# Optimization experiments

Hardware: AMD Instinct MI355X
Metric: run time of the kernel (lower is better)

Reference implementation:

```python
import jax, jax.numpy as jnp
import numpy as np

EMB = 256   # EMB_SIZE hard-coded in source
H = 8       # num heads (all heads share the same Q/K/V, as in source)
DK = EMB // H  # 32
B, T = 16, 2048
LN_EPS = 1e-5


def _layernorm(a, g, b):
    m = jnp.mean(a, axis=-1, keepdims=True)
    v = jnp.mean(jnp.square(a - m), axis=-1, keepdims=True)
    return (a - m) * jax.lax.rsqrt(v + LN_EPS) * g + b


def setup_inputs() -> dict:
    key = jax.random.key(0)
    ks = jax.random.split(key, 8)
    sc = 0.02
    return {
        "x": jax.random.normal(ks[0], (B, T, EMB), jnp.float32),
        "Wq": jax.random.normal(ks[1], (EMB, DK), jnp.float32) * sc,
        "Wk": jax.random.normal(ks[2], (EMB, DK), jnp.float32) * sc,
        "Wv": jax.random.normal(ks[3], (EMB, DK), jnp.float32) * sc,
        "Wp": jax.random.normal(ks[4], (EMB, EMB), jnp.float32) * sc,
        "bp": jnp.zeros((EMB,), jnp.float32),
        "W1": jax.random.normal(ks[5], (EMB, 4 * EMB), jnp.float32) * sc,
        "b1": jnp.zeros((4 * EMB,), jnp.float32),
        "W2": jax.random.normal(ks[6], (4 * EMB, EMB), jnp.float32) * sc,
        "b2": jnp.zeros((EMB,), jnp.float32),
        "g1": jnp.ones((EMB,), jnp.float32),
        "be1": jnp.zeros((EMB,), jnp.float32),
        "g2": jnp.ones((EMB,), jnp.float32),
        "be2": jnp.zeros((EMB,), jnp.float32),
    }


def reference(x, Wq, Wk, Wv, Wp, bp, W1, b1, W2, b2, g1, be1, g2, be2):
    # Single shared-head QKV projections (bias-free), as in source
    q = x @ Wq  # [B,T,DK]
    k = x @ Wk
    v = x @ Wv
    # Causal self-attention with explicit score matrix [B,T,T]
    scores = jnp.einsum("btd,bsd->bts", q, k) / jnp.sqrt(jnp.float32(DK))
    causal = jnp.tril(jnp.ones((T, T), dtype=bool))
    scores = jnp.where(causal, scores, -jnp.inf)
    a = jax.nn.softmax(scores, axis=-1)
    attn = jnp.einsum("bts,bsd->btd", a, v)  # [B,T,DK]
    # Source concatenates h identical copies of the same attention output
    cat = jnp.tile(attn, (1, 1, H))  # [B,T,EMB]
    mh = cat @ Wp + bp
    y1 = _layernorm(x + mh, g1, be1)
    ff = jax.nn.gelu(y1 @ W1 + b1, approximate=False) @ W2 + b2
    return _layernorm(y1 + ff, g2, be2)
```

## Files before the change

### kernel.cpp

```cpp
#include <hip/hip_runtime.h>

#define BB 16
#define TT 2048
#define EE 256
#define DK 32
#define MM (BB*TT)
#define FF 1024

typedef __bf16 bf16_t;
typedef __bf16 bf16x8 __attribute__((ext_vector_type(8)));
typedef __bf16 bf16x4 __attribute__((ext_vector_type(4)));
typedef float  f32x4  __attribute__((ext_vector_type(4)));

__device__ __forceinline__ f32x4 mfma16(bf16x8 a, bf16x8 b, f32x4 c){
  return __builtin_amdgcn_mfma_f32_16x16x32_bf16(a, b, c, 0, 0, 0);
}
__device__ __forceinline__ void gload_lds16(const void* g, void* l){
  __builtin_amdgcn_global_load_lds((__attribute__((address_space(1))) void*)g,
                                   (__attribute__((address_space(3))) void*)l,
                                   16, 0, 0);
}

__launch_bounds__(256)
__global__ void prep_kernel(const float* __restrict__ Wq, const float* __restrict__ Wk,
                            const float* __restrict__ Wv, const float* __restrict__ Wp,
                            const float* __restrict__ W1, const float* __restrict__ W2,
                            bf16_t* __restrict__ wqkv, float* __restrict__ wpe,
                            bf16_t* __restrict__ w1t, bf16_t* __restrict__ w2t)
{
  const int i = blockIdx.x*256 + threadIdx.x;
  if (i < 96*256) {
    const int r = i >> 8, c = i & 255;
    float v;
    if (r < 32)      v = Wq[c*32 + r] * 0.17677669529663687f;
    else if (r < 64) v = Wk[c*32 + (r-32)];
    else             v = Wv[c*32 + (r-64)];
    wqkv[i] = (bf16_t)v;
  }
  if (i < 32*256) {
    const int d = i >> 8, n = i & 255;
    float s = 0.f;
    #pragma unroll
    for (int h = 0; h < 8; ++h) s += Wp[(h*32 + d)*256 + n];
    wpe[i] = s;
  }
  if (i < 1024*256) {
    const int n = i >> 8, k = i & 255;
    w1t[i] = (bf16_t)W1[(size_t)k*1024 + n];
  }
  if (i < 256*1024) {
    const int n = i >> 10, k = i & 1023;
    w2t[i] = (bf16_t)W2[(size_t)k*256 + n];
  }
}

__launch_bounds__(256)
__global__ void qkv_kernel(const float* __restrict__ x, const bf16_t* __restrict__ wqkv,
                           bf16_t* __restrict__ q, bf16_t* __restrict__ kd,
                           bf16_t* __restrict__ vT)
{
  __shared__ bf16_t Ws[96*256];
  bf16_t* Vt = Ws;
  const int tid = threadIdx.x;
  #pragma unroll
  for (int i = 0; i < 12; ++i) {
    const int v8  = tid + i*256;
    const int row = v8 >> 5;
    const int bir = (v8 & 31) * 16;
    *(bf16x8*)((char*)Ws + row*512 + (bir ^ ((row & 7) << 4))) =
        *(const bf16x8*)(wqkv + (size_t)v8*8);
  }
  __syncthreads();

  const int w = tid >> 6, l = tid & 63;
  const int lr = l & 15, lk4 = l >> 4, lkb = lk4*8;
  const int m0 = blockIdx.x * 64;
  const int arow = m0 + w*16 + lr;
  const float* xr = x + (size_t)arow * 256;

  f32x4 acc[6] = {};
  #pragma unroll
  for (int s = 0; s < 8; ++s) {
    const int kb = s*32 + lkb;
    const float4 v0 = *(const float4*)(xr + kb);
    const float4 v1 = *(const float4*)(xr + kb + 4);
    bf16x8 a;
    a[0]=(bf16_t)v0.x; a[1]=(bf16_t)v0.y; a[2]=(bf16_t)v0.z; a[3]=(bf16_t)v0.w;
    a[4]=(bf16_t)v1.x; a[5]=(bf16_t)v1.y; a[6]=(bf16_t)v1.z; a[7]=(bf16_t)v1.w;
    #pragma unroll
    for (int j = 0; j < 6; ++j) {
      const int nrow = j*16 + lr;
      const bf16x8 bf = *(const bf16x8*)((const char*)Ws + nrow*512 +
                                         ((kb*2) ^ ((nrow & 7) << 4)));
      acc[j] = mfma16(a, bf, acc[j]);
    }
  }
  #pragma unroll
  for (int j = 0; j < 4; ++j) {
    #pragma unroll
    for (int r = 0; r < 4; ++r) {
      const int orow = m0 + w*16 + lk4*4 + r;
      const int col  = j*16 + lr;
      const bf16_t v = (bf16_t)acc[j][r];
      if (col < 32) q[(size_t)orow*32 + col] = v;
      else          kd[(size_t)orow*32 + (col-32)] = v;
    }
  }
  __syncthreads();
  #pragma unroll
  for (int j = 4; j < 6; ++j)
    #pragma unroll
    for (int r = 0; r < 4; ++r) {
      const int d = (j-4)*16 + lr;
      const int t = w*16 + lk4*4 + r;
      *(bf16_t*)((char*)Vt + d*128 + ((((t>>3) ^ (d&7))<<4) | ((t&7)*2))) =
          (bf16_t)acc[j][r];
    }
  __syncthreads();
  {
    const int d = tid >> 3, c8 = tid & 7;
    const bf16x8 v = *(const bf16x8*)((char*)Vt + d*128 + ((c8 ^ (d&7))<<4));
    *(bf16x8*)(vT + ((size_t)(m0 >> 11)*32 + d)*TT + (m0 & 2047) + c8*8) = v;
  }
}

__launch_bounds__(256)
__global__ void attnp_kernel(const bf16_t* __restrict__ q, const bf16_t* __restrict__ kd,
                             const bf16_t* __restrict__ vT,
                             float* __restrict__ part_acc, float* __restrict__ part_ml)
{
  __shared__ bf16_t P[4][16*128];
  const int tid = threadIdx.x;
  const int w = tid >> 6, l = tid & 63;
  const int wv = blockIdx.x*4 + w;
  const int lr = l & 15, g4 = l >> 4;
  const float NEG_INF = -__builtin_inff();

  const int b = wv / 320;
  const int u = wv - b*320;
  int r, base;
  if      (u >= 192) { r = 3; base = 192; }
  else if (u >= 96)  { r = 2; base = 96;  }
  else if (u >= 32)  { r = 1; base = 32;  }
  else               { r = 0; base = 0;   }
  const int qq = u - base;
  const int g  = r*32 + qq / (r+1);
  const int c  = qq - (qq / (r+1))*(r+1);
  const int t_total = (g >> 3) + 1;
  const int t0 = c*4;
  const int t1 = min(t0 + 4, t_total);

  const bf16_t* qb = q  + (size_t)b*TT*32;
  const bf16_t* kb = kd + (size_t)b*TT*32;
  const bf16_t* vb = vT + (size_t)b*32*TT;
  const int q0 = g*16;
  const int qg = q0 + lr;

  const bf16x8 qa = *(const bf16x8*)(qb + (size_t)(q0 + lr)*32 + g4*8);
  const bf16_t* v0r = vb + (size_t)lr*TT;
  const bf16_t* v1r = vb + (size_t)(16 + lr)*TT;

  f32x4 acc0 = {0.f,0.f,0.f,0.f}, acc1 = {0.f,0.f,0.f,0.f};
  float mrun = NEG_INF, lsum = 0.f;
  char* pb = (char*)&P[w][0];
  const int swz = (lr & 7) << 4;
  const f32x4 zf = {0.f,0.f,0.f,0.f};

  for (int t = t0; t < t1; ++t) {
    const int k0 = t * 128;
    f32x4 s[8];
    #pragma unroll
    for (int cc = 0; cc < 8; ++cc) {
      const bf16x8 kf = *(const bf16x8*)(kb + (size_t)(k0 + cc*16 + lr)*32 + g4*8);
      s[cc] = mfma16(kf, qa, zf);
    }
    if (t == t_total - 1) {
      #pragma unroll
      for (int cc = 0; cc < 8; ++cc)
        #pragma unroll
        for (int rr = 0; rr < 4; ++rr)
          if (k0 + cc*16 + g4*4 + rr > qg) s[cc][rr] = NEG_INF;
    }
    float mt = NEG_INF;
    #pragma unroll
    for (int cc = 0; cc < 8; ++cc) {
      float a01 = fmaxf(s[cc][0], s[cc][1]), a23 = fmaxf(s[cc][2], s[cc][3]);
      mt = fmaxf(mt, fmaxf(a01, a23));
    }
    mt = fmaxf(mt, __shfl_xor(mt, 16));
    mt = fmaxf(mt, __shfl_xor(mt, 32));
    const float mn = fmaxf(mrun, mt);
    const float sc = __expf(mrun - mn);
    float ps = 0.f;
    #pragma unroll
    for (int cc = 0; cc < 8; ++cc) {
      float p0 = __expf(s[cc][0]-mn), p1 = __expf(s[cc][1]-mn);
      float p2 = __expf(s[cc][2]-mn), p3 = __expf(s[cc][3]-mn);
      s[cc][0]=p0; s[cc][1]=p1; s[cc][2]=p2; s[cc][3]=p3;
      ps += (p0+p1) + (p2+p3);
    }
    ps += __shfl_xor(ps, 16);
    ps += __shfl_xor(ps, 32);
    lsum = lsum*sc + ps;
    mrun = mn;
    acc0 *= sc; acc1 *= sc;
    #pragma unroll
    for (int cc = 0; cc < 8; ++cc) {
      bf16x4 pk;
      pk[0]=(bf16_t)s[cc][0]; pk[1]=(bf16_t)s[cc][1];
      pk[2]=(bf16_t)s[cc][2]; pk[3]=(bf16_t)s[cc][3];
      *(bf16x4*)(pb + lr*256 + ((cc*32 + g4*8) ^ swz)) = pk;
    }
    #pragma unroll
    for (int h = 0; h < 4; ++h) {
      const bf16x8 pbf = *(const bf16x8*)(pb + lr*256 + ((h*64 + g4*16) ^ swz));
      acc0 = mfma16(*(const bf16x8*)(v0r + k0 + h*32 + g4*8), pbf, acc0);
      acc1 = mfma16(*(const bf16x8*)(v1r + k0 + h*32 + g4*8), pbf, acc1);
    }
  }
  float* pa = part_acc + (size_t)wv*512;
  *(f32x4*)(pa + l*8)     = acc0;
  *(f32x4*)(pa + l*8 + 4) = acc1;
  if (l < 16) {
    part_ml[wv*32 + l]      = mrun;
    part_ml[wv*32 + 16 + l] = lsum;
  }
}

__launch_bounds__(256)
__global__ void attnc_kernel(const float* __restrict__ part_acc,
                             const float* __restrict__ part_ml,
                             bf16_t* __restrict__ attn)
{
  const int tid = threadIdx.x;
  const int id = blockIdx.x*4 + (tid >> 6);
  const int l = tid & 63, lr = l & 15, g4 = l >> 4;
  const int b = id >> 7, g = id & 127;
  const int r = g >> 5;
  const int base = (r == 0) ? 0 : (r == 1) ? 32 : (r == 2) ? 96 : 192;
  const int p0 = b*320 + base + (g - (r << 5))*(r + 1);
  const int nc = r + 1;
  const float NEG_INF = -__builtin_inff();

  float m0v=NEG_INF,m1v=NEG_INF,m2v=NEG_INF,m3v=NEG_INF;
  float l0v=0,l1v=0,l2v=0,l3v=0;
  f32x4 a00={0,0,0,0},a01={0,0,0,0},a10={0,0,0,0},a11={0,0,0,0};
  f32x4 a20={0,0,0,0},a21={0,0,0,0},a30={0,0,0,0},a31={0,0,0,0};
  {
    const float* pa = part_acc + (size_t)p0*512;
    a00 = *(const f32x4*)(pa + l*8); a01 = *(const f32x4*)(pa + l*8 + 4);
    m0v = part_ml[p0*32 + lr]; l0v = part_ml[p0*32 + 16 + lr];
  }
  if (nc > 1) {
    const float* pa = part_acc + (size_t)(p0+1)*512;
    a10 = *(const f32x4*)(pa + l*8); a11 = *(const f32x4*)(pa + l*8 + 4);
    m1v = part_ml[(p0+1)*32 + lr]; l1v = part_ml[(p0+1)*32 + 16 + lr];
  }
  if (nc > 2) {
    const float* pa = part_acc + (size_t)(p0+2)*512;
    a20 = *(const f32x4*)(pa + l*8); a21 = *(const f32x4*)(pa + l*8 + 4);
    m2v = part_ml[(p0+2)*32 + lr]; l2v = part_ml[(p0+2)*32 + 16 + lr];
  }
  if (nc > 3) {
    const float* pa = part_acc + (size_t)(p0+3)*512;
    a30 = *(const f32x4*)(pa + l*8); a31 = *(const f32x4*)(pa + l*8 + 4);
    m3v = part_ml[(p0+3)*32 + lr]; l3v = part_ml[(p0+3)*32 + 16 + lr];
  }
  const float M = fmaxf(fmaxf(m0v, m1v), fmaxf(m2v, m3v));
  const float w0 = __expf(m0v - M), w1 = __expf(m1v - M);
  const float w2 = __expf(m2v - M), w3 = __expf(m3v - M);
  const float L = l0v*w0 + l1v*w1 + l2v*w2 + l3v*w3;
  const float inv = 1.0f / L;
  f32x4 o0 = (a00*w0 + a10*w1 + a20*w2 + a30*w3) * inv;
  f32x4 o1 = (a01*w0 + a11*w1 + a21*w2 + a31*w3) * inv;

  bf16_t* ao = attn + ((size_t)b*TT + g*16 + lr)*32;
  bf16x4 ob0, ob1;
  ob0[0]=(bf16_t)o0[0]; ob0[1]=(bf16_t)o0[1]; ob0[2]=(bf16_t)o0[2]; ob0[3]=(bf16_t)o0[3];
  ob1[0]=(bf16_t)o1[0]; ob1[1]=(bf16_t)o1[1]; ob1[2]=(bf16_t)o1[2]; ob1[3]=(bf16_t)o1[3];
  *(bf16x4*)(ao + g4*4)      = ob0;
  *(bf16x4*)(ao + 16 + g4*4) = ob1;
}

__launch_bounds__(256)
__global__ void ln1_kernel(const float* __restrict__ x, const bf16_t* __restrict__ attn,
                           const float* __restrict__ wpe, const float* __restrict__ bp,
                           const float* __restrict__ g1, const float* __restrict__ be1,
                           bf16_t* __restrict__ y1b)
{
  __shared__ float Wp_s[32*256];
  const int tid = threadIdx.x;
  for (int i = tid; i < 32*64; i += 256)
    ((float4*)Wp_s)[i] = ((const float4*)wpe)[i];
  __syncthreads();

  const int w = tid >> 6, l = tid & 63;
  const int n = l * 4;
  const float4 gv  = *(const float4*)(g1  + n);
  const float4 bev = *(const float4*)(be1 + n);
  const float4 bpv = *(const float4*)(bp  + n);

  #pragma unroll 1
  for (int it = 0; it < 8; ++it) {
    const int row = blockIdx.x*32 + it*4 + w;
    const bf16_t* ar = attn + (size_t)row*32;
    float a[32];
    #pragma unroll
    for (int i = 0; i < 4; ++i) {
      const bf16x8 t = *(const bf16x8*)(ar + i*8);
      #pragma unroll
      for (int j = 0; j < 8; ++j) a[i*8 + j] = (float)t[j];
    }
    float mh[4] = {bpv.x, bpv.y, bpv.z, bpv.w};
    #pragma unroll
    for (int d = 0; d < 32; ++d) {
      const float4 wv = *(const float4*)(Wp_s + d*256 + n);
      const float ad = a[d];
      mh[0] = fmaf(ad, wv.x, mh[0]); mh[1] = fmaf(ad, wv.y, mh[1]);
      mh[2] = fmaf(ad, wv.z, mh[2]); mh[3] = fmaf(ad, wv.w, mh[3]);
    }
    const float4 xv = *(const float4*)(x + (size_t)row*256 + n);
    const float t0 = xv.x + mh[0], t1 = xv.y + mh[1];
    const float t2 = xv.z + mh[2], t3 = xv.w + mh[3];
    float s1 = (t0+t1) + (t2+t3);
    float s2 = (t0*t0 + t1*t1) + (t2*t2 + t3*t3);
    #pragma unroll
    for (int m = 1; m < 64; m <<= 1) { s1 += __shfl_xor(s1, m); s2 += __shfl_xor(s2, m); }
    const float mean = s1 * (1.0f/256.0f);
    const float var  = s2 * (1.0f/256.0f) - mean*mean;
    const float rs   = rsqrtf(var + 1e-5f);
    float4 yv;
    yv.x = (t0-mean)*rs*gv.x + bev.x; yv.y = (t1-mean)*rs*gv.y + bev.y;
    yv.z = (t2-mean)*rs*gv.z + bev.z; yv.w = (t3-mean)*rs*gv.w + bev.w;
    bf16x4 yb; yb[0]=(bf16_t)yv.x; yb[1]=(bf16_t)yv.y; yb[2]=(bf16_t)yv.z; yb[3]=(bf16_t)yv.w;
    *(bf16x4*)(y1b + (size_t)row*256 + n) = yb;
  }
}

__launch_bounds__(512, 1)
__global__ void mlp_kernel(const bf16_t* __restrict__ y1b, const bf16_t* __restrict__ w1t,
                           const float* __restrict__ b1, const bf16_t* __restrict__ w2t,
                           const float* __restrict__ b2, const float* __restrict__ g2,
                           const float* __restrict__ be2, float* __restrict__ out)
{
  __shared__ char SM[135168];
  const int tid = threadIdx.x;
  const int w = tid >> 6, l = tid & 63;
  const int lr = l & 15, g4 = l >> 4;
  const int m0 = blockIdx.x * 128;
  const int rw = w & 3;
  const int cw = w >> 2;
  const int wm  = rw * 32;
  const int wn1 = cw * 16;
  const int wn2 = cw * 128;

  {
    const float2 bv = *(const float2*)(b1 + tid*2);
    *(float2*)(SM + 131072 + tid*8) = bv;
  }
  bf16x8 aA[2][8];
  #pragma unroll
  for (int t = 0; t < 2; ++t)
    #pragma unroll
    for (int kk = 0; kk < 8; ++kk)
      aA[t][kk] = *(const bf16x8*)(y1b +
          (size_t)(m0 + wm + t*16 + lr)*256 + kk*32 + g4*8);
  asm volatile("s_waitcnt vmcnt(0) lgkmcnt(0)" ::: "memory");
  __builtin_amdgcn_sched_barrier(0);

  #define ST_W1(c, s)                                                         \
    { _Pragma("unroll")                                                       \
      for (int p_ = 0; p_ < 2; ++p_) {                                        \
        const int idx_ = p_*512 + tid;                                        \
        const int r_ = idx_ >> 5, c_ = idx_ & 31;                             \
        const int sc_ = (c_ & 24) | ((c_ ^ r_) & 7);                          \
        gload_lds16(w1t + (size_t)((c)*32 + r_)*256 + sc_*8,                  \
                    SM + (s)*16384 + idx_*16);                                \
      } }
  #define ST_W2(c, s)                                                         \
    { _Pragma("unroll")                                                       \
      for (int p_ = 0; p_ < 2; ++p_) {                                        \
        const int idx_ = p_*512 + tid;                                        \
        const int r_ = idx_ >> 2, c_ = idx_ & 3;                              \
        gload_lds16(w2t + (size_t)r_*1024 + (c)*32 + ((c_ ^ r_) & 3)*8,       \
                    SM + 49152 + (s)*16384 + idx_*16);                        \
      } }

  ST_W1(0, 0);
  ST_W1(1, 1);
  ST_W2(0, 0);

  f32x4 oacc[2][8] = {};

  #pragma unroll 1
  for (int i = 0; i < 32; ++i) {
    if (i < 31) { asm volatile("s_waitcnt vmcnt(4)" ::: "memory"); }
    else        { asm volatile("s_waitcnt vmcnt(2)" ::: "memory"); }
    __builtin_amdgcn_sched_barrier(0);
    asm volatile("s_waitcnt lgkmcnt(0)" ::: "memory");
    __builtin_amdgcn_sched_barrier(0);
    __builtin_amdgcn_s_barrier();
    __builtin_amdgcn_sched_barrier(0);

    const char* sw1 = SM + (i % 3)*16384;
    f32x4 ah[2] = {};
    const int nr = wn1 + lr;
    __builtin_amdgcn_s_setprio(1);
    #pragma unroll
    for (int kk = 0; kk < 8; ++kk) {
      const bf16x8 bf = *(const bf16x8*)(sw1 + nr*512 +
                                         ((kk*64 + g4*16) ^ ((nr & 7) << 4)));
      ah[0] = mfma16(aA[0][kk], bf, ah[0]);
      ah[1] = mfma16(aA[1][kk], bf, ah[1]);
    }
    if (i > 0) {
      const char* sw2 = SM + 49152 + ((i-1) % 3)*16384;
      const char* hs  = SM + 98304 + ((i-1) & 1)*16384;
      bf16x8 ha[2], wb[8];
      #pragma unroll
      for (int i3 = 0; i3 < 2; ++i3) {
        const int row = wm + i3*16 + lr;
        ha[i3] = *(const bf16x8*)(hs + row*128 + ((g4*16) ^ ((row & 7) << 4)));
      }
      #pragma unroll
      for (int j3 = 0; j3 < 8; ++j3) {
        const int n = wn2 + j3*16 + lr;
        wb[j3] = *(const bf16x8*)(sw2 + n*64 + ((g4*16) ^ ((n & 3) << 4)));
      }
      #pragma unroll
      for (int i3 = 0; i3 < 2; ++i3)
        #pragma unroll
        for (int j3 = 0; j3 < 8; ++j3)
          oacc[i3][j3] = mfma16(ha[i3], wb[j3], oacc[i3][j3]);
    }
    __builtin_amdgcn_s_setprio(0);
    {
      const float bias = *(const float*)(SM + 131072 + (i*32 + wn1 + lr)*4);
      char* hw = SM + 98304 + (i & 1)*16384;
      const int hc2 = (wn1 + lr)*2;
      #pragma unroll
      for (int i3 = 0; i3 < 2; ++i3)
        #pragma unroll
        for (int r = 0; r < 4; ++r) {
          const int hrow = wm + i3*16 + g4*4 + r;
          const float v = ah[i3][r] + bias;
          const float z = 1.5957691216057308f * v * fmaf(0.044715f, v*v, 1.0f);
          const float gg = v * __builtin_amdgcn_rcpf(1.0f + __expf(-z));
          *(bf16_t*)(hw + hrow*128 + (hc2 ^ ((hrow & 7) << 4))) = (bf16_t)gg;
        }
    }
    if (i <= 29) ST_W1(i+2, (i+2) % 3);
    if (i <= 30) ST_W2(i+1, (i+1) % 3);
  }
  #undef ST_W1
  #undef ST_W2

  asm volatile("s_waitcnt vmcnt(0)" ::: "memory");
  __builtin_amdgcn_sched_barrier(0);
  asm volatile("s_waitcnt lgkmcnt(0)" ::: "memory");
  __builtin_amdgcn_sched_barrier(0);
  __builtin_amdgcn_s_barrier();
  __builtin_amdgcn_sched_barrier(0);
  {
    const char* sw2 = SM + 49152 + (31 % 3)*16384;
    const char* hs  = SM + 98304 + (31 & 1)*16384;
    bf16x8 ha[2], wb[8];
    #pragma unroll
    for (int i3 = 0; i3 < 2; ++i3) {
      const int row = wm + i3*16 + lr;
      ha[i3] = *(const bf16x8*)(hs + row*128 + ((g4*16) ^ ((row & 7) << 4)));
    }
    #pragma unroll
    for (int j3 = 0; j3 < 8; ++j3) {
      const int n = wn2 + j3*16 + lr;
      wb[j3] = *(const bf16x8*)(sw2 + n*64 + ((g4*16) ^ ((n & 3) << 4)));
    }
    #pragma unroll
    for (int i3 = 0; i3 < 2; ++i3)
      #pragma unroll
      for (int j3 = 0; j3 < 8; ++j3)
        oacc[i3][j3] = mfma16(ha[i3], wb[j3], oacc[i3][j3]);
  }

  float b2r[8], g2r[8], be2r[8];
  #pragma unroll
  for (int j3 = 0; j3 < 8; ++j3) {
    const int col = wn2 + j3*16 + lr;
    b2r[j3] = b2[col]; g2r[j3] = g2[col]; be2r[j3] = be2[col];
  }
  #pragma unroll
  for (int i3 = 0; i3 < 2; ++i3)
    #pragma unroll
    for (int r = 0; r < 4; ++r) {
      const int grow = m0 + wm + i3*16 + g4*4 + r;
      #pragma unroll
      for (int j3 = 0; j3 < 8; ++j3) {
        const int col = wn2 + j3*16 + lr;
        oacc[i3][j3][r] += b2r[j3] + (float)y1b[(size_t)grow*256 + col];
      }
    }
  __syncthreads();
  float* red = (float*)SM;
  #pragma unroll
  for (int i3 = 0; i3 < 2; ++i3)
    #pragma unroll
    for (int r = 0; r < 4; ++r) {
      float s1 = 0.f, s2 = 0.f;
      #pragma unroll
      for (int j3 = 0; j3 < 8; ++j3) {
        s1 += oacc[i3][j3][r]; s2 += oacc[i3][j3][r]*oacc[i3][j3][r];
      }
      #pragma unroll
      for (int m = 1; m < 16; m <<= 1) { s1 += __shfl_xor(s1, m); s2 += __shfl_xor(s2, m); }
      if (lr == 0) {
        const int rl = wm + i3*16 + g4*4 + r;
        red[rl*4 + cw*2]     = s1;
        red[rl*4 + cw*2 + 1] = s2;
      }
    }
  __syncthreads();
  #pragma unroll
  for (int i3 = 0; i3 < 2; ++i3)
    #pragma unroll
    for (int r = 0; r < 4; ++r) {
      const int rl = wm + i3*16 + g4*4 + r;
      const float S1 = red[rl*4+0] + red[rl*4+2];
      const float S2 = red[rl*4+1] + red[rl*4+3];
      const float mean = S1 * (1.0f/256.0f);
      const float var  = S2 * (1.0f/256.0f) - mean*mean;
      const float rs   = rsqrtf(var + 1e-5f);
      #pragma unroll
      for (int j3 = 0; j3 < 8; ++j3) {
        const int col = wn2 + j3*16 + lr;
        out[(size_t)(m0 + rl)*256 + col] = (oacc[i3][j3][r] - mean)*rs*g2r[j3] + be2r[j3];
      }
    }
}

extern "C" void kernel_launch(void* const* d_in, const int* in_sizes, int n_in,
                              void* d_out, int out_size, void* d_ws, size_t ws_size,
                              hipStream_t stream)
{
  const float* x   = (const float*)d_in[0];
  const float* Wq  = (const float*)d_in[1];
  const float* Wk  = (const float*)d_in[2];
  const float* Wv  = (const float*)d_in[3];
  const float* Wp  = (const float*)d_in[4];
  const float* bp  = (const float*)d_in[5];
  const float* W1  = (const float*)d_in[6];
  const float* b1  = (const float*)d_in[7];
  const float* W2  = (const float*)d_in[8];
  const float* b2  = (const float*)d_in[9];
  const float* g1  = (const float*)d_in[10];
  const float* be1 = (const float*)d_in[11];
  const float* g2  = (const float*)d_in[12];
  const float* be2 = (const float*)d_in[13];

  char* ws = (char*)d_ws;
  bf16_t* qd   = (bf16_t*)(ws + ((size_t)0  << 20));
  bf16_t* kd   = (bf16_t*)(ws + ((size_t)2  << 20));
  bf16_t* vTd  = (bf16_t*)(ws + ((size_t)4  << 20));
  bf16_t* attn = (bf16_t*)(ws + ((size_t)6  << 20));
  bf16_t* y1b  = (bf16_t*)(ws + ((size_t)8  << 20));
  bf16_t* wqkv = (bf16_t*)(ws + ((size_t)24 << 20));
  float*  wpe  = (float*) (ws + ((size_t)25 << 20));
  bf16_t* w1t  = (bf16_t*)(ws + ((size_t)26 << 20));
  bf16_t* w2t  = (bf16_t*)(ws + ((size_t)27 << 20));
  float*  pml  = (float*) (ws + ((size_t)28 << 20));
  float*  pacc = (float*) (ws + ((size_t)29 << 20));
  float* out = (float*)d_out;

  prep_kernel<<<1024, 256, 0, stream>>>(Wq, Wk, Wv, Wp, W1, W2, wqkv, wpe, w1t, w2t);
  qkv_kernel<<<512, 256, 0, stream>>>(x, wqkv, qd, kd, vTd);
  attnp_kernel<<<1280, 256, 0, stream>>>(qd, kd, vTd, pacc, pml);
  attnc_kernel<<<512, 256, 0, stream>>>(pacc, pml, attn);
  ln1_kernel<<<1024, 256, 0, stream>>>(x, attn, wpe, bp, g1, be1, y1b);
  mlp_kernel<<<256, 512, 0, stream>>>(y1b, w1t, b1, w2t, b2, g2, be2, out);
}
```

Measured before the change: 133.2 us.

## Halve MLP block tile to 64 rows, two blocks per CU, simpler double-buffer pipeline

The fused MLP kernel now uses 64-row tiles with 256 threads and 72KB LDS, so two blocks can share a CU and 512 blocks cover more CUs than the previous 256. The software pipeline drops from a three-stage W1 prefetch with a skewed GEMM2 to a plain double buffer with in-iteration GELU. The hidden tile is single-buffered behind an extra barrier, and the first GEMM's operands are swapped so GELU output is written as bf16x4 vectors. This trades deeper prefetch and more weight reuse per block for higher occupancy and better CU coverage, at the cost of twice the weight traffic and more barriers.

Result: no change. 135.3 us (+1.6%).

```diff
diff --git a/kernel.cpp b/kernel.cpp
--- a/kernel.cpp
+++ b/kernel.cpp
@@ -337,26 +337,26 @@
   }
 }
 
-__launch_bounds__(512, 1)
+__launch_bounds__(256, 2)
 __global__ void mlp_kernel(const bf16_t* __restrict__ y1b, const bf16_t* __restrict__ w1t,
                            const float* __restrict__ b1, const bf16_t* __restrict__ w2t,
                            const float* __restrict__ b2, const float* __restrict__ g2,
                            const float* __restrict__ be2, float* __restrict__ out)
 {
-  __shared__ char SM[135168];
+  __shared__ char SM[73728];
   const int tid = threadIdx.x;
   const int w = tid >> 6, l = tid & 63;
   const int lr = l & 15, g4 = l >> 4;
-  const int m0 = blockIdx.x * 128;
-  const int rw = w & 3;
-  const int cw = w >> 2;
-  const int wm  = rw * 32;
+  const int m0 = blockIdx.x * 64;
+  const int rw = w >> 1;
+  const int cw = w & 1;
+  const int mb  = rw * 32;
   const int wn1 = cw * 16;
   const int wn2 = cw * 128;
 
   {
-    const float2 bv = *(const float2*)(b1 + tid*2);
-    *(float2*)(SM + 131072 + tid*8) = bv;
+    const float4 bv = *(const float4*)(b1 + tid*4);
+    *(float4*)(SM + 69632 + tid*16) = bv;
   }
   bf16x8 aA[2][8];
   #pragma unroll
@@ -364,14 +364,14 @@
     #pragma unroll
     for (int kk = 0; kk < 8; ++kk)
       aA[t][kk] = *(const bf16x8*)(y1b +
-          (size_t)(m0 + wm + t*16 + lr)*256 + kk*32 + g4*8);
+          (size_t)(m0 + mb + t*16 + lr)*256 + kk*32 + g4*8);
   asm volatile("s_waitcnt vmcnt(0) lgkmcnt(0)" ::: "memory");
   __builtin_amdgcn_sched_barrier(0);
 
   #define ST_W1(c, s)                                                         \
     { _Pragma("unroll")                                                       \
-      for (int p_ = 0; p_ < 2; ++p_) {                                        \
-        const int idx_ = p_*512 + tid;                                        \
+      for (int p_ = 0; p_ < 4; ++p_) {                                        \
+        const int idx_ = p_*256 + tid;                                        \
         const int r_ = idx_ >> 5, c_ = idx_ & 31;                             \
         const int sc_ = (c_ & 24) | ((c_ ^ r_) & 7);                          \
         gload_lds16(w1t + (size_t)((c)*32 + r_)*256 + sc_*8,                  \
@@ -379,48 +379,65 @@
       } }
   #define ST_W2(c, s)                                                         \
     { _Pragma("unroll")                                                       \
-      for (int p_ = 0; p_ < 2; ++p_) {                                        \
-        const int idx_ = p_*512 + tid;                                        \
+      for (int p_ = 0; p_ < 4; ++p_) {                                        \
+        const int idx_ = p_*256 + tid;                                        \
         const int r_ = idx_ >> 2, c_ = idx_ & 3;                              \
         gload_lds16(w2t + (size_t)r_*1024 + (c)*32 + ((c_ ^ r_) & 3)*8,       \
-                    SM + 49152 + (s)*16384 + idx_*16);                        \
+                    SM + 32768 + (s)*16384 + idx_*16);                        \
       } }
 
   ST_W1(0, 0);
-  ST_W1(1, 1);
   ST_W2(0, 0);
 
   f32x4 oacc[2][8] = {};
+  char* hb = SM + 65536;
 
   #pragma unroll 1
   for (int i = 0; i < 32; ++i) {
-    if (i < 31) { asm volatile("s_waitcnt vmcnt(4)" ::: "memory"); }
-    else        { asm volatile("s_waitcnt vmcnt(2)" ::: "memory"); }
+    asm volatile("s_waitcnt vmcnt(0)" ::: "memory");
     __builtin_amdgcn_sched_barrier(0);
+    __builtin_amdgcn_s_barrier();
+    __builtin_amdgcn_sched_barrier(0);
+
+    const char* sw1 = SM + (i & 1)*16384;
+    f32x4 ah[2] = {};
+    __builtin_amdgcn_s_setprio(1);
+    #pragma unroll
+    for (int kk = 0; kk < 8; ++kk) {
+      const int row = wn1 + lr;
+      const bf16x8 wf = *(const bf16x8*)(sw1 + row*512 +
+                                         ((kk*64 + g4*16) ^ ((row & 7) << 4)));
+      ah[0] = mfma16(wf, aA[0][kk], ah[0]);
+      ah[1] = mfma16(wf, aA[1][kk], ah[1]);
+    }
+    __builtin_amdgcn_s_setprio(0);
+    {
+      const float4 bias = *(const float4*)(SM + 69632 + (i*32 + wn1 + g4*4)*4);
+      #pragma unroll
+      for (int t = 0; t < 2; ++t) {
+        const int m = mb + t*16 + lr;
+        bf16x4 hv;
+        #pragma unroll
+        for (int r = 0; r < 4; ++r) {
+          const float v = ah[t][r] + bias[r];
+          const float z = 1.5957691216057308f * v * fmaf(0.044715f, v*v, 1.0f);
+          hv[r] = (bf16_t)(v * __builtin_amdgcn_rcpf(1.0f + __expf(-z)));
+        }
+        *(bf16x4*)(hb + m*64 + (((wn1 + g4*4)*2) ^ ((m & 3) << 4))) = hv;
+      }
+    }
     asm volatile("s_waitcnt lgkmcnt(0)" ::: "memory");
     __builtin_amdgcn_sched_barrier(0);
     __builtin_amdgcn_s_barrier();
     __builtin_amdgcn_sched_barrier(0);
-
-    const char* sw1 = SM + (i % 3)*16384;
-    f32x4 ah[2] = {};
-    const int nr = wn1 + lr;
+    const char* sw2 = SM + 32768 + (i & 1)*16384;
     __builtin_amdgcn_s_setprio(1);
-    #pragma unroll
-    for (int kk = 0; kk < 8; ++kk) {
-      const bf16x8 bf = *(const bf16x8*)(sw1 + nr*512 +
-                                         ((kk*64 + g4*16) ^ ((nr & 7) << 4)));
-      ah[0] = mfma16(aA[0][kk], bf, ah[0]);
-      ah[1] = mfma16(aA[1][kk], bf, ah[1]);
-    }
-    if (i > 0) {
-      const char* sw2 = SM + 49152 + ((i-1) % 3)*16384;
-      const char* hs  = SM + 98304 + ((i-1) & 1)*16384;
+    {
       bf16x8 ha[2], wb[8];
       #pragma unroll
       for (int i3 = 0; i3 < 2; ++i3) {
-        const int row = wm + i3*16 + lr;
-        ha[i3] = *(const bf16x8*)(hs + row*128 + ((g4*16) ^ ((row & 7) << 4)));
+        const int row = mb + i3*16 + lr;
+        ha[i3] = *(const bf16x8*)(hb + row*64 + ((g4*16) ^ ((row & 3) << 4)));
       }
       #pragma unroll
       for (int j3 = 0; j3 < 8; ++j3) {
@@ -434,53 +451,10 @@
           oacc[i3][j3] = mfma16(ha[i3], wb[j3], oacc[i3][j3]);
     }
     __builtin_amdgcn_s_setprio(0);
-    {
-      const float bias = *(const float*)(SM + 131072 + (i*32 + wn1 + lr)*4);
-      char* hw = SM + 98304 + (i & 1)*16384;
-      const int hc2 = (wn1 + lr)*2;
-      #pragma unroll
-      for (int i3 = 0; i3 < 2; ++i3)
-        #pragma unroll
-        for (int r = 0; r < 4; ++r) {
-          const int hrow = wm + i3*16 + g4*4 + r;
-          const float v = ah[i3][r] + bias;
-          const float z = 1.5957691216057308f * v * fmaf(0.044715f, v*v, 1.0f);
-          const float gg = v * __builtin_amdgcn_rcpf(1.0f + __expf(-z));
-          *(bf16_t*)(hw + hrow*128 + (hc2 ^ ((hrow & 7) << 4))) = (bf16_t)gg;
-        }
-    }
-    if (i <= 29) ST_W1(i+2, (i+2) % 3);
-    if (i <= 30) ST_W2(i+1, (i+1) % 3);
+    if (i < 31) { ST_W1(i+1, (i+1)&1); ST_W2(i+1, (i+1)&1); }
   }
   #undef ST_W1
   #undef ST_W2
-
-  asm volatile("s_waitcnt vmcnt(0)" ::: "memory");
-  __builtin_amdgcn_sched_barrier(0);
-  asm volatile("s_waitcnt lgkmcnt(0)" ::: "memory");
-  __builtin_amdgcn_sched_barrier(0);
-  __builtin_amdgcn_s_barrier();
-  __builtin_amdgcn_sched_barrier(0);
-  {
-    const char* sw2 = SM + 49152 + (31 % 3)*16384;
-    const char* hs  = SM + 98304 + (31 & 1)*16384;
-    bf16x8 ha[2], wb[8];
-    #pragma unroll
-    for (int i3 = 0; i3 < 2; ++i3) {
-      const int row = wm + i3*16 + lr;
-      ha[i3] = *(const bf16x8*)(hs + row*128 + ((g4*16) ^ ((row & 7) << 4)));
-    }
-    #pragma unroll
-    for (int j3 = 0; j3 < 8; ++j3) {
-      const int n = wn2 + j3*16 + lr;
-      wb[j3] = *(const bf16x8*)(sw2 + n*64 + ((g4*16) ^ ((n & 3) << 4)));
-    }
-    #pragma unroll
-    for (int i3 = 0; i3 < 2; ++i3)
-      #pragma unroll
-      for (int j3 = 0; j3 < 8; ++j3)
-        oacc[i3][j3] = mfma16(ha[i3], wb[j3], oacc[i3][j3]);
-  }
 
   float b2r[8], g2r[8], be2r[8];
   #pragma unroll
@@ -492,7 +466,7 @@
   for (int i3 = 0; i3 < 2; ++i3)
     #pragma unroll
     for (int r = 0; r < 4; ++r) {
-      const int grow = m0 + wm + i3*16 + g4*4 + r;
+      const int grow = m0 + mb + i3*16 + g4*4 + r;
       #pragma unroll
       for (int j3 = 0; j3 < 8; ++j3) {
         const int col = wn2 + j3*16 + lr;
@@ -513,7 +487,7 @@
       #pragma unroll
       for (int m = 1; m < 16; m <<= 1) { s1 += __shfl_xor(s1, m); s2 += __shfl_xor(s2, m); }
       if (lr == 0) {
-        const int rl = wm + i3*16 + g4*4 + r;
+        const int rl = mb + i3*16 + g4*4 + r;
         red[rl*4 + cw*2]     = s1;
         red[rl*4 + cw*2 + 1] = s2;
       }
@@ -523,7 +497,7 @@
   for (int i3 = 0; i3 < 2; ++i3)
     #pragma unroll
     for (int r = 0; r < 4; ++r) {
-      const int rl = wm + i3*16 + g4*4 + r;
+      const int rl = mb + i3*16 + g4*4 + r;
       const float S1 = red[rl*4+0] + red[rl*4+2];
       const float S2 = red[rl*4+1] + red[rl*4+3];
       const float mean = S1 * (1.0f/256.0f);
@@ -575,5 +549,5 @@
   attnp_kernel<<<1280, 256, 0, stream>>>(qd, kd, vTd, pacc, pml);
   attnc_kernel<<<512, 256, 0, stream>>>(pacc, pml, attn);
   ln1_kernel<<<1024, 256, 0, stream>>>(x, attn, wpe, bp, g1, be1, y1b);
-  mlp_kernel<<<256, 512, 0, stream>>>(y1b, w1t, b1, w2t, b2, g2, be2, out);
-}
+  mlp_kernel<<<512, 256, 0, stream>>>(y1b, w1t, b1, w2t, b2, g2, be2, out);
+}
```
